# Optimization experiments

Measured on AMD Instinct MI355X. Metric: run time of the kernel, lower is better.

## Reference

```python
import jax, jax.numpy as jnp
import numpy as np

NUM_ITER = 5
DIM = 512
BATCH = 64


def setup_inputs() -> dict:
    key = jax.random.key(0)
    a = jax.random.normal(key, (BATCH, DIM, DIM), dtype=jnp.float32)
    # Symmetric PSD input (covariance-like), as in bilinear pooling; Newton-Schulz
    # requires SPD matrices for convergence.
    x = jnp.einsum('bik,bjk->bij', a, a) / DIM
    I = jnp.eye(DIM, dtype=jnp.float32)
    return {"x": x, "I": I}


def reference(x, I):
    # x: [bs, dim, dim]; I: [dim, dim]
    normA = jnp.sqrt(jnp.sum(x * x, axis=(1, 2), keepdims=True))  # Frobenius norm per matrix
    Y = x / normA
    bs, dim, _ = x.shape
    Z = jnp.broadcast_to(I, (bs, dim, dim))
    Ib = Z
    for _ in range(NUM_ITER):
        T = 0.5 * (3.0 * Ib - jnp.matmul(Z, Y))
        Y = jnp.matmul(Y, T)
        Z = jnp.matmul(T, Z)
    sA = Y * jnp.sqrt(normA)
    return sA
```

## Files before the change

kernel.cpp:

```cpp
#include <hip/hip_runtime.h>
#include <hip/hip_bf16.h>
#include <stdint.h>

#define DIM   512
#define BATCH 64
#define KENC  1024
#define BM    256
#define BN    256
#define BKT   32
#define NKT   16
#define BUFE  32768

typedef __attribute__((ext_vector_type(8))) short short8;
typedef __attribute__((ext_vector_type(4))) float floatx4;

__device__ __forceinline__ ushort f2bf(float f) {
    __hip_bfloat16 h = __float2bfloat16(f);
    return *(ushort*)&h;
}
__device__ __forceinline__ float bf2f(ushort u) {
    __hip_bfloat16 h = *(__hip_bfloat16*)&u;
    return (float)h;
}

typedef __attribute__((address_space(3))) uint32_t lds_u32;
typedef const __attribute__((address_space(1))) uint32_t glb_u32;
__device__ __forceinline__ void gload16(const ushort* g, ushort* l) {
    __builtin_amdgcn_global_load_lds((glb_u32*)g, (lds_u32*)l, 16, 0, 0);
}

__global__ __launch_bounds__(256) void norm_partial_kernel(const float* __restrict__ x,
                                                           float* __restrict__ partial) {
    int b = blockIdx.y;
    int i = blockIdx.x;
    const float4* xv = (const float4*)(x + (size_t)b * DIM * DIM + (size_t)i * (DIM * DIM / 16));
    float s = 0.f;
    #pragma unroll
    for (int r = 0; r < 16; ++r) {
        float4 v = xv[r * 256 + threadIdx.x];
        s += v.x * v.x + v.y * v.y + v.z * v.z + v.w * v.w;
    }
    #pragma unroll
    for (int off = 32; off > 0; off >>= 1) s += __shfl_down(s, off, 64);
    __shared__ float red[4];
    int lane = threadIdx.x & 63, wid = threadIdx.x >> 6;
    if (lane == 0) red[wid] = s;
    __syncthreads();
    if (threadIdx.x == 0) partial[b * 16 + i] = red[0] + red[1] + red[2] + red[3];
}

__global__ __launch_bounds__(256) void init_kernel(const float* __restrict__ x,
                                                   const float* __restrict__ partial,
                                                   float* __restrict__ norms,
                                                   ushort* __restrict__ Yenc,
                                                   ushort* __restrict__ Tenc) {
    int b = blockIdx.y;
    float s = 0.f;
    #pragma unroll
    for (int p = 0; p < 16; ++p) s += partial[b * 16 + p];
    float nrm = sqrtf(s);
    if (blockIdx.x == 0 && threadIdx.x == 0) norms[b] = nrm;
    float inv = 1.0f / nrm;
    int idx = (blockIdx.x * 256 + threadIdx.x) * 4;
    int r = idx >> 9;
    int c = idx & 511;
    float4 v = *(const float4*)(x + (size_t)b * DIM * DIM + idx);
    float yv[4] = {v.x * inv, v.y * inv, v.z * inv, v.w * inv};
    size_t base = (size_t)b * DIM * KENC + (size_t)r * KENC;
    ushort yhi[4], ylo[4], thi[4], tlo[4];
    #pragma unroll
    for (int j = 0; j < 4; ++j) {
        float y = yv[j];
        yhi[j] = f2bf(y);
        ylo[j] = f2bf(y - bf2f(yhi[j]));
        float t = ((c + j) == r ? 1.5f : 0.0f) - 0.5f * y;
        thi[j] = f2bf(t);
        tlo[j] = f2bf(t - bf2f(thi[j]));
    }
    *(ushort4*)(Yenc + base + c)       = *(ushort4*)yhi;
    *(ushort4*)(Yenc + base + 512 + c) = *(ushort4*)ylo;
    *(ushort4*)(Tenc + base + c)       = *(ushort4*)thi;
    *(ushort4*)(Tenc + base + 512 + c) = *(ushort4*)tlo;
}

__device__ __forceinline__ void stage_tile(ushort* buf, const ushort* Ag, const ushort* Bg,
                                           int k0, int tid) {
    int row = tid >> 2;
    int pc  = tid & 3;
    int kc  = ((pc ^ ((row >> 1) & 3)) << 3);
    const ushort* ar = Ag + (size_t)row * KENC + k0 + kc;
    const ushort* br = Bg + (size_t)row * KENC + k0 + kc;
    gload16(ar,       &buf[tid * 8]);
    gload16(ar + 512, &buf[8192 + tid * 8]);
    gload16(br,       &buf[16384 + tid * 8]);
    gload16(br + 512, &buf[24576 + tid * 8]);
}

__device__ __forceinline__ void compute_tile(const ushort* buf, floatx4 (&acc)[4][4],
                                             int wrow, int wcol, int lane15, int fo) {
    const ushort* Ash = buf;
    const ushort* Asl = buf + 8192;
    const ushort* Bsh = buf + 16384;
    const ushort* Bsl = buf + 24576;
    short8 ah[4], bh[4], xl[4];
    #pragma unroll
    for (int i = 0; i < 4; ++i)
        ah[i] = *(const short8*)&Ash[(wrow + i * 16 + lane15) * BKT + fo];
    #pragma unroll
    for (int j = 0; j < 4; ++j)
        bh[j] = *(const short8*)&Bsh[(wcol + j * 16 + lane15) * BKT + fo];
    #pragma unroll
    for (int i = 0; i < 4; ++i)
        #pragma unroll
        for (int j = 0; j < 4; ++j)
            acc[i][j] = __builtin_amdgcn_mfma_f32_16x16x32_bf16(ah[i], bh[j], acc[i][j], 0, 0, 0);
    #pragma unroll
    for (int j = 0; j < 4; ++j)
        xl[j] = *(const short8*)&Bsl[(wcol + j * 16 + lane15) * BKT + fo];
    #pragma unroll
    for (int i = 0; i < 4; ++i)
        #pragma unroll
        for (int j = 0; j < 4; ++j)
            acc[i][j] = __builtin_amdgcn_mfma_f32_16x16x32_bf16(ah[i], xl[j], acc[i][j], 0, 0, 0);
    #pragma unroll
    for (int i = 0; i < 4; ++i)
        xl[i] = *(const short8*)&Asl[(wrow + i * 16 + lane15) * BKT + fo];
    #pragma unroll
    for (int i = 0; i < 4; ++i)
        #pragma unroll
        for (int j = 0; j < 4; ++j)
            acc[i][j] = __builtin_amdgcn_mfma_f32_16x16x32_bf16(xl[i], bh[j], acc[i][j], 0, 0, 0);
}

__device__ __forceinline__ void store_enc(ushort* Cenc, size_t matoff, int gr, int gc, float v) {
    ushort hi = f2bf(v);
    ushort lo = f2bf(v - bf2f(hi));
    Cenc[matoff + (size_t)gr * KENC + gc] = hi;
    Cenc[matoff + (size_t)gr * KENC + 512 + gc] = lo;
}

template <int MODE>
__global__ __launch_bounds__(1024, 4) void gemm_bt(const ushort* __restrict__ A,
                                                   const ushort* __restrict__ B,
                                                   ushort* __restrict__ Cenc,
                                                   float* __restrict__ Cout,
                                                   const float* __restrict__ norms) {
    __shared__ __attribute__((aligned(16))) ushort sm[2 * BUFE];

    int f = blockIdx.x;
    int xcd = f & 7;
    int g   = f >> 3;
    int b   = xcd + 8 * (g >> 2);
    int t   = g & 3;
    int bm  = t >> 1;
    int bn  = t & 1;

    size_t matoff = (size_t)b * DIM * KENC;
    const ushort* Ag = A + matoff + (size_t)bm * BM * KENC;
    const ushort* Bg = B + matoff + (size_t)bn * BN * KENC;

    int tid = threadIdx.x;
    int wave = tid >> 6, lane = tid & 63;
    int lane15 = lane & 15, quad = lane >> 4;
    int wrow = (wave >> 2) * 64, wcol = (wave & 3) * 64;
    int s2 = (lane15 >> 1) & 3;
    int fo = ((quad ^ s2) << 3);

    floatx4 acc[4][4];
    #pragma unroll
    for (int i = 0; i < 4; ++i)
        #pragma unroll
        for (int j = 0; j < 4; ++j)
            acc[i][j] = (floatx4){0.f, 0.f, 0.f, 0.f};

    stage_tile(sm, Ag, Bg, 0, tid);
    for (int kt = 0; kt < NKT; ++kt) {
        ushort* cur = sm + (kt & 1) * BUFE;
        ushort* nxt = sm + ((kt + 1) & 1) * BUFE;
        __syncthreads();
        if (kt + 1 < NKT) stage_tile(nxt, Ag, Bg, (kt + 1) * BKT, tid);
        compute_tile(cur, acc, wrow, wcol, lane15, fo);
    }

    float scale = (MODE == 2) ? sqrtf(norms[b]) : 0.f;
    #pragma unroll
    for (int i = 0; i < 4; ++i) {
        int gr0 = bm * BM + wrow + i * 16 + quad * 4;
        #pragma unroll
        for (int j = 0; j < 4; ++j) {
            int gc = bn * BN + wcol + j * 16 + lane15;
            #pragma unroll
            for (int rr = 0; rr < 4; ++rr) {
                int gr = gr0 + rr;
                float cv = acc[i][j][rr];
                if (MODE == 0) {
                    store_enc(Cenc, matoff, gr, gc, (gr == gc ? 1.5f : 0.0f) - 0.5f * cv);
                } else if (MODE == 1) {
                    store_enc(Cenc, matoff, gr, gc, cv);
                } else {
                    Cout[(size_t)b * DIM * DIM + (size_t)gr * DIM + gc] = cv * scale;
                }
            }
        }
    }
}

extern "C" void kernel_launch(void* const* d_in, const int* in_sizes, int n_in,
                              void* d_out, int out_size, void* d_ws, size_t ws_size,
                              hipStream_t stream) {
    const float* x = (const float*)d_in[0];
    float* out = (float*)d_out;

    const size_t MATB = (size_t)BATCH * DIM * KENC * sizeof(ushort);
    char* ws = (char*)d_ws;
    ushort* W0 = (ushort*)(ws + 0 * MATB);
    ushort* W1 = (ushort*)(ws + 1 * MATB);
    ushort* W2 = (ushort*)(ws + 2 * MATB);
    float* partial = (float*)(ws + 3 * MATB);
    float* norms   = (float*)(ws + 3 * MATB + 4096);
    ushort* D = (ushort*)d_out;

    dim3 gblk(1024);
    dim3 g1(256);

    norm_partial_kernel<<<dim3(16, BATCH), 256, 0, stream>>>(x, partial);
    init_kernel<<<dim3(256, BATCH), 256, 0, stream>>>(x, partial, norms, W0, W1);

    gemm_bt<1><<<g1, gblk, 0, stream>>>(W0, W1, W2, nullptr, nullptr);
    gemm_bt<0><<<g1, gblk, 0, stream>>>(W1, W2, W0, nullptr, nullptr);
    gemm_bt<1><<<g1, gblk, 0, stream>>>(W2, W0, D, nullptr, nullptr);
    gemm_bt<1><<<g1, gblk, 0, stream>>>(W0, W1, W2, nullptr, nullptr);
    gemm_bt<0><<<g1, gblk, 0, stream>>>(W2, D, W0, nullptr, nullptr);
    gemm_bt<1><<<g1, gblk, 0, stream>>>(D, W0, W1, nullptr, nullptr);
    gemm_bt<1><<<g1, gblk, 0, stream>>>(W0, W2, D, nullptr, nullptr);
    gemm_bt<0><<<g1, gblk, 0, stream>>>(D, W1, W0, nullptr, nullptr);
    gemm_bt<1><<<g1, gblk, 0, stream>>>(W1, W0, W2, nullptr, nullptr);
    gemm_bt<1><<<g1, gblk, 0, stream>>>(W0, D, W1, nullptr, nullptr);
    gemm_bt<0><<<g1, gblk, 0, stream>>>(W1, W2, W0, nullptr, nullptr);
    gemm_bt<2><<<g1, gblk, 0, stream>>>(W2, W0, nullptr, out, norms);
}
```

Before: 839.8 us.

## Use 512-thread blocks with 128x64 warp tiles and split hi/lo staged pipeline

```diff
diff --git a/kernel.cpp b/kernel.cpp
--- a/kernel.cpp
+++ b/kernel.cpp
@@ -28,6 +28,9 @@
 __device__ __forceinline__ void gload16(const ushort* g, ushort* l) {
     __builtin_amdgcn_global_load_lds((glb_u32*)g, (lds_u32*)l, 16, 0, 0);
 }
+
+#define WAITVM(N) asm volatile("s_waitcnt vmcnt(" #N ")" ::: "memory")
+#define BARRIER() do { __builtin_amdgcn_s_barrier(); __builtin_amdgcn_sched_barrier(0); } while (0)
 
 __global__ __launch_bounds__(256) void norm_partial_kernel(const float* __restrict__ x,
                                                            float* __restrict__ partial) {
@@ -83,53 +86,33 @@
     *(ushort4*)(Tenc + base + 512 + c) = *(ushort4*)tlo;
 }
 
-__device__ __forceinline__ void stage_tile(ushort* buf, const ushort* Ag, const ushort* Bg,
-                                           int k0, int tid) {
-    int row = tid >> 2;
-    int pc  = tid & 3;
-    int kc  = ((pc ^ ((row >> 1) & 3)) << 3);
-    const ushort* ar = Ag + (size_t)row * KENC + k0 + kc;
-    const ushort* br = Bg + (size_t)row * KENC + k0 + kc;
-    gload16(ar,       &buf[tid * 8]);
-    gload16(ar + 512, &buf[8192 + tid * 8]);
-    gload16(br,       &buf[16384 + tid * 8]);
-    gload16(br + 512, &buf[24576 + tid * 8]);
-}
-
-__device__ __forceinline__ void compute_tile(const ushort* buf, floatx4 (&acc)[4][4],
-                                             int wrow, int wcol, int lane15, int fo) {
-    const ushort* Ash = buf;
-    const ushort* Asl = buf + 8192;
-    const ushort* Bsh = buf + 16384;
-    const ushort* Bsl = buf + 24576;
-    short8 ah[4], bh[4], xl[4];
-    #pragma unroll
-    for (int i = 0; i < 4; ++i)
-        ah[i] = *(const short8*)&Ash[(wrow + i * 16 + lane15) * BKT + fo];
-    #pragma unroll
-    for (int j = 0; j < 4; ++j)
-        bh[j] = *(const short8*)&Bsh[(wcol + j * 16 + lane15) * BKT + fo];
-    #pragma unroll
-    for (int i = 0; i < 4; ++i)
-        #pragma unroll
-        for (int j = 0; j < 4; ++j)
-            acc[i][j] = __builtin_amdgcn_mfma_f32_16x16x32_bf16(ah[i], bh[j], acc[i][j], 0, 0, 0);
-    #pragma unroll
-    for (int j = 0; j < 4; ++j)
-        xl[j] = *(const short8*)&Bsl[(wcol + j * 16 + lane15) * BKT + fo];
-    #pragma unroll
-    for (int i = 0; i < 4; ++i)
-        #pragma unroll
-        for (int j = 0; j < 4; ++j)
-            acc[i][j] = __builtin_amdgcn_mfma_f32_16x16x32_bf16(ah[i], xl[j], acc[i][j], 0, 0, 0);
-    #pragma unroll
-    for (int i = 0; i < 4; ++i)
-        xl[i] = *(const short8*)&Asl[(wrow + i * 16 + lane15) * BKT + fo];
-    #pragma unroll
-    for (int i = 0; i < 4; ++i)
-        #pragma unroll
-        for (int j = 0; j < 4; ++j)
-            acc[i][j] = __builtin_amdgcn_mfma_f32_16x16x32_bf16(xl[i], bh[j], acc[i][j], 0, 0, 0);
+__device__ __forceinline__ void stage_hi(ushort* buf, const ushort* Ag, const ushort* Bg,
+                                         int k0, int tid) {
+    #pragma unroll
+    for (int s = 0; s < 2; ++s) {
+        int vt = tid + s * 512;
+        int row = vt >> 2;
+        int pc  = vt & 3;
+        int kc  = ((pc ^ ((row >> 1) & 3)) << 3);
+        const ushort* ar = Ag + (size_t)row * KENC + k0 + kc;
+        const ushort* br = Bg + (size_t)row * KENC + k0 + kc;
+        gload16(ar, &buf[vt * 8]);
+        gload16(br, &buf[16384 + vt * 8]);
+    }
+}
+__device__ __forceinline__ void stage_lo(ushort* buf, const ushort* Ag, const ushort* Bg,
+                                         int k0, int tid) {
+    #pragma unroll
+    for (int s = 0; s < 2; ++s) {
+        int vt = tid + s * 512;
+        int row = vt >> 2;
+        int pc  = vt & 3;
+        int kc  = ((pc ^ ((row >> 1) & 3)) << 3);
+        const ushort* ar = Ag + (size_t)row * KENC + k0 + kc;
+        const ushort* br = Bg + (size_t)row * KENC + k0 + kc;
+        gload16(ar + 512, &buf[8192 + vt * 8]);
+        gload16(br + 512, &buf[24576 + vt * 8]);
+    }
 }
 
 __device__ __forceinline__ void store_enc(ushort* Cenc, size_t matoff, int gr, int gc, float v) {
@@ -140,11 +123,11 @@
 }
 
 template <int MODE>
-__global__ __launch_bounds__(1024, 4) void gemm_bt(const ushort* __restrict__ A,
-                                                   const ushort* __restrict__ B,
-                                                   ushort* __restrict__ Cenc,
-                                                   float* __restrict__ Cout,
-                                                   const float* __restrict__ norms) {
+__global__ __launch_bounds__(512, 2) void gemm_bt(const ushort* __restrict__ A,
+                                                  const ushort* __restrict__ B,
+                                                  ushort* __restrict__ Cenc,
+                                                  float* __restrict__ Cout,
+                                                  const float* __restrict__ norms) {
     __shared__ __attribute__((aligned(16))) ushort sm[2 * BUFE];
 
     int f = blockIdx.x;
@@ -162,29 +145,89 @@
     int tid = threadIdx.x;
     int wave = tid >> 6, lane = tid & 63;
     int lane15 = lane & 15, quad = lane >> 4;
-    int wrow = (wave >> 2) * 64, wcol = (wave & 3) * 64;
+    int wrow = (wave >> 2) * 128;
+    int wcol = (wave & 3) * 64;
     int s2 = (lane15 >> 1) & 3;
     int fo = ((quad ^ s2) << 3);
 
-    floatx4 acc[4][4];
-    #pragma unroll
-    for (int i = 0; i < 4; ++i)
+    floatx4 acc[8][4];
+    #pragma unroll
+    for (int i = 0; i < 8; ++i)
         #pragma unroll
         for (int j = 0; j < 4; ++j)
             acc[i][j] = (floatx4){0.f, 0.f, 0.f, 0.f};
 
-    stage_tile(sm, Ag, Bg, 0, tid);
+    stage_hi(sm, Ag, Bg, 0, tid);
+    stage_lo(sm, Ag, Bg, 0, tid);
+    WAITVM(4);
+    BARRIER();
+
+    #pragma unroll 2
     for (int kt = 0; kt < NKT; ++kt) {
-        ushort* cur = sm + (kt & 1) * BUFE;
+        const ushort* cur = sm + (kt & 1) * BUFE;
         ushort* nxt = sm + ((kt + 1) & 1) * BUFE;
-        __syncthreads();
-        if (kt + 1 < NKT) stage_tile(nxt, Ag, Bg, (kt + 1) * BKT, tid);
-        compute_tile(cur, acc, wrow, wcol, lane15, fo);
+        const ushort* Ash = cur;
+        const ushort* Asl = cur + 8192;
+        const ushort* Bsh = cur + 16384;
+        const ushort* Bsl = cur + 24576;
+
+        short8 ab[8], bb[4], xl[4];
+
+        #pragma unroll
+        for (int i = 0; i < 8; ++i)
+            ab[i] = *(const short8*)&Ash[(wrow + i * 16 + lane15) * BKT + fo];
+        #pragma unroll
+        for (int j = 0; j < 4; ++j)
+            bb[j] = *(const short8*)&Bsh[(wcol + j * 16 + lane15) * BKT + fo];
+        if (kt + 1 < NKT) {
+            stage_hi(nxt, Ag, Bg, (kt + 1) * BKT, tid);
+            WAITVM(4);
+        } else {
+            WAITVM(0);
+        }
+        BARRIER();
+        __builtin_amdgcn_s_setprio(1);
+        #pragma unroll
+        for (int i = 0; i < 8; ++i)
+            #pragma unroll
+            for (int j = 0; j < 4; ++j)
+                acc[i][j] = __builtin_amdgcn_mfma_f32_16x16x32_bf16(ab[i], bb[j], acc[i][j], 0, 0, 0);
+        __builtin_amdgcn_s_setprio(0);
+        BARRIER();
+
+        #pragma unroll
+        for (int j = 0; j < 4; ++j)
+            xl[j] = *(const short8*)&Bsl[(wcol + j * 16 + lane15) * BKT + fo];
+        if (kt + 1 < NKT)
+            stage_lo(nxt, Ag, Bg, (kt + 1) * BKT, tid);
+        BARRIER();
+        __builtin_amdgcn_s_setprio(1);
+        #pragma unroll
+        for (int i = 0; i < 8; ++i)
+            #pragma unroll
+            for (int j = 0; j < 4; ++j)
+                acc[i][j] = __builtin_amdgcn_mfma_f32_16x16x32_bf16(ab[i], xl[j], acc[i][j], 0, 0, 0);
+        __builtin_amdgcn_s_setprio(0);
+        BARRIER();
+
+        #pragma unroll
+        for (int i = 0; i < 8; ++i)
+            ab[i] = *(const short8*)&Asl[(wrow + i * 16 + lane15) * BKT + fo];
+        BARRIER();
+        __builtin_amdgcn_s_setprio(1);
+        #pragma unroll
+        for (int i = 0; i < 8; ++i)
+            #pragma unroll
+            for (int j = 0; j < 4; ++j)
+                acc[i][j] = __builtin_amdgcn_mfma_f32_16x16x32_bf16(ab[i], bb[j], acc[i][j], 0, 0, 0);
+        __builtin_amdgcn_s_setprio(0);
+        if (kt + 1 < NKT) WAITVM(4);
+        BARRIER();
     }
 
     float scale = (MODE == 2) ? sqrtf(norms[b]) : 0.f;
     #pragma unroll
-    for (int i = 0; i < 4; ++i) {
+    for (int i = 0; i < 8; ++i) {
         int gr0 = bm * BM + wrow + i * 16 + quad * 4;
         #pragma unroll
         for (int j = 0; j < 4; ++j) {
@@ -220,7 +263,7 @@
     float* norms   = (float*)(ws + 3 * MATB + 4096);
     ushort* D = (ushort*)d_out;
 
-    dim3 gblk(1024);
+    dim3 gblk(512);
     dim3 g1(256);
 
     norm_partial_kernel<<<dim3(16, BATCH), 256, 0, stream>>>(x, partial);
```

Result: faster. 752.4 us (-10.4%).
